# Performance work log

Measured on AMD Instinct MI355X. Metric: run time of the kernel, lower is better.

## Reference

```python
import jax, jax.numpy as jnp
import numpy as np

EMBED_DIM = 1024
NUM_HEADS = 16
N_QUBITS = 4
CIRCUIT_DEPTH = 2


def setup_inputs() -> dict:
    key = jax.random.key(0)
    ks = jax.random.split(key, 6)
    B, S, E = 2, 2048, EMBED_DIM
    x = jax.random.normal(ks[0], (B, S, E), dtype=jnp.float32)
    Wq = jax.random.normal(ks[1], (E, E), dtype=jnp.float32) / np.sqrt(E)
    Wk = jax.random.normal(ks[2], (E, E), dtype=jnp.float32) / np.sqrt(E)
    Wv = jax.random.normal(ks[3], (E, E), dtype=jnp.float32) / np.sqrt(E)
    Wo = jax.random.normal(ks[4], (E, E), dtype=jnp.float32) / np.sqrt(E)
    q_params = jax.random.normal(ks[5], (N_QUBITS, CIRCUIT_DEPTH), dtype=jnp.float32)
    return {"x": x, "Wq": Wq, "Wk": Wk, "Wv": Wv, "Wo": Wo, "q_params": q_params}


def reference(x, Wq, Wk, Wv, Wo, q_params):
    B, S, E = x.shape
    H, dk = NUM_HEADS, E // NUM_HEADS
    # QKV projections (Linear, no bias): y = x @ W.T
    q = (x @ Wq.T).reshape(B, S, H, dk).transpose(0, 2, 1, 3)  # [B,H,S,dk]
    k = (x @ Wk.T).reshape(B, S, H, dk).transpose(0, 2, 1, 3)
    v = (x @ Wv.T).reshape(B, S, H, dk).transpose(0, 2, 1, 3)
    scores = jnp.einsum("bhqd,bhkd->bhqk", q, k) / jnp.sqrt(jnp.float32(dk))
    attn = jax.nn.softmax(scores, axis=-1)
    classical = jnp.einsum("bhqk,bhkd->bhqd", attn, v)  # [B,H,S,dk]
    # Quantum circuit collapses analytically: RX-only circuit, <Z_0> depends
    # only on the rotations on wire 0 -> cos(sum_depth q_params[0, :]).
    c = jnp.cos(jnp.sum(q_params[0, :]))
    mixed = classical.at[..., :N_QUBITS].add(c)
    mixed = mixed.transpose(0, 2, 1, 3).reshape(B, S, E)
    return mixed @ Wo.T
```

## Files before the change

### kernel.cpp

```cpp
#include <hip/hip_runtime.h>

typedef unsigned short u16;
typedef unsigned int u32;
typedef __attribute__((ext_vector_type(8))) short short8;
typedef __attribute__((ext_vector_type(8))) _Float16 half8;
typedef __attribute__((ext_vector_type(4))) float f32x4;
typedef __attribute__((ext_vector_type(16))) float f32x16;
typedef __attribute__((ext_vector_type(4))) u32 u32x4;

#define S_LEN 2048
#define EDIM  1024
#define DK    64
#define NHEAD 16
#define QSCALE 0.1803368801111f

__device__ inline u16 f2bf(float f) {
    u32 u = __builtin_bit_cast(u32, f);
    u += 0x7fffu + ((u >> 16) & 1u);
    return (u16)(u >> 16);
}
__device__ inline u16 f2h(float f) {
    _Float16 h = (_Float16)f;
    return __builtin_bit_cast(u16, h);
}

#define ASYNC16(gp, lp)                                                        \
    __builtin_amdgcn_global_load_lds(                                          \
        (const __attribute__((address_space(1))) u32*)(gp),                    \
        (__attribute__((address_space(3))) u32*)(lp), 16, 0, 0)

__global__ __launch_bounds__(256)
void conv_all(const float* __restrict__ x,  const float* __restrict__ Wq,
              const float* __restrict__ Wk, const float* __restrict__ Wv,
              u16* __restrict__ xb, u16* __restrict__ Wb ) {
    const int blk = blockIdx.x;
    const float* src; u16* dst; int idx;
    if (blk < 4096)      { src = x;  dst = xb;             idx = blk; }
    else if (blk < 5120) { src = Wq; dst = Wb;             idx = blk - 4096; }
    else if (blk < 6144) { src = Wk; dst = Wb + (1 << 20); idx = blk - 5120; }
    else                 { src = Wv; dst = Wb + (2 << 20); idx = blk - 6144; }
    const int i = idx * 1024 + threadIdx.x * 4;
    const float4 v = *(const float4*)(src + i);
    u16 o[4] = { f2bf(v.x), f2bf(v.y), f2bf(v.z), f2bf(v.w) };
    *(ulong1*)(dst + i) = *(ulong1*)o;
}

__global__ __launch_bounds__(256)
void f32_to_bf16(const float* __restrict__ src, u16* __restrict__ dst, int n) {
    const int i = (blockIdx.x * 256 + threadIdx.x) * 4;
    if (i + 3 < n) {
        const float4 v = *(const float4*)(src + i);
        u16 o[4] = { f2bf(v.x), f2bf(v.y), f2bf(v.z), f2bf(v.w) };
        *(ulong1*)(dst + i) = *(ulong1*)o;
    }
}

template<int EPI, bool BF32, int MT>
__global__ __launch_bounds__(256, 2)
void gemm128(const u16* __restrict__ A,
             const void* __restrict__ B0, const void* __restrict__ B1,
             const void* __restrict__ B2,
             u16* __restrict__ C0, u16* __restrict__ C1, u16* __restrict__ C2,
             float* __restrict__ Cf, int M, int N, int K) {
    const void* Bv = B0;
    u16*        Cp = C0;
    float       cscale = (EPI == 0) ? QSCALE : 1.0f;
    if (blockIdx.z == 1) { Bv = B1; Cp = C1; cscale = 1.0f; }
    else if (blockIdx.z == 2) { Bv = B2; Cp = C2; cscale = 1.0f; }

    const int tid  = threadIdx.x;
    const int lane = tid & 63;
    const int w    = tid >> 6;
    const int quad = lane >> 4;
    const int l16  = lane & 15;
    const int wm   = w >> 1;
    const int wn   = w & 1;
    const int m0   = blockIdx.y * (MT * 32);
    const int n0   = blockIdx.x * 128;

    __shared__ u16 lA[MT * 32 * 32];
    __shared__ __align__(16) char lBraw[BF32 ? 128 * 32 * 4 : 128 * 32 * 2];

    f32x4 acc[MT][4] = {};

    for (int k0 = 0; k0 < K; k0 += 32) {
        __syncthreads();
#pragma unroll
        for (int i = 0; i < MT / 2; ++i) {
            const int row = w * (MT * 8) + i * 16 + (lane >> 2);
            const int col = (lane & 3) * 8;
            ASYNC16(A + (size_t)(m0 + row) * K + k0 + col,
                    &lA[(w * (MT * 8) + i * 16) * 32]);
        }
        if (BF32) {
            const float* Bp = (const float*)Bv;
            float*       lB = (float*)lBraw;
#pragma unroll
            for (int i = 0; i < 4; ++i) {
                const int row = w * 32 + i * 8 + (lane >> 3);
                const int col = (lane & 7) * 4;
                ASYNC16(Bp + (size_t)(n0 + row) * K + k0 + col,
                        &lB[(w * 32 + i * 8) * 32]);
            }
        } else {
            const u16* Bp = (const u16*)Bv;
            u16*       lB = (u16*)lBraw;
#pragma unroll
            for (int i = 0; i < 2; ++i) {
                const int row = w * 32 + i * 16 + (lane >> 2);
                const int col = (lane & 3) * 8;
                ASYNC16(Bp + (size_t)(n0 + row) * K + k0 + col,
                        &lB[(w * 32 + i * 16) * 32]);
            }
        }
        __syncthreads();

        short8 av[MT], bv[4];
#pragma unroll
        for (int t = 0; t < MT; ++t)
            av[t] = *(const short8*)&lA[(wm * (MT * 16) + t * 16 + l16) * 32 + quad * 8];
        if (BF32) {
            const float* lB = (const float*)lBraw;
#pragma unroll
            for (int t = 0; t < 4; ++t) {
                const float* src = &lB[(wn * 64 + t * 16 + l16) * 32 + quad * 8];
                const f32x4 x0 = *(const f32x4*)src;
                const f32x4 x1 = *(const f32x4*)(src + 4);
                short8 bq;
#pragma unroll
                for (int j = 0; j < 4; ++j) {
                    bq[j]     = (short)f2bf(x0[j]);
                    bq[4 + j] = (short)f2bf(x1[j]);
                }
                bv[t] = bq;
            }
        } else {
            const u16* lB = (const u16*)lBraw;
#pragma unroll
            for (int t = 0; t < 4; ++t)
                bv[t] = *(const short8*)&lB[(wn * 64 + t * 16 + l16) * 32 + quad * 8];
        }

#pragma unroll
        for (int mt = 0; mt < MT; ++mt)
#pragma unroll
            for (int nt = 0; nt < 4; ++nt)
                acc[mt][nt] = __builtin_amdgcn_mfma_f32_16x16x32_bf16(
                    av[mt], bv[nt], acc[mt][nt], 0, 0, 0);
    }

#pragma unroll
    for (int mt = 0; mt < MT; ++mt)
#pragma unroll
        for (int nt = 0; nt < 4; ++nt) {
            if (EPI == 0 && blockIdx.z == 2) {
                const int col  = n0 + wn * 64 + nt * 16 + l16;
                const int h    = (col >> 6) & 15;
                const int d    = col & 63;
                const int rowb = m0 + wm * (MT * 16) + mt * 16 + quad * 4;
                const int b    = rowb >> 11;
                const int s    = rowb & 2047;
                ushort4 o;
                o.x = f2h(acc[mt][nt][0]);
                o.y = f2h(acc[mt][nt][1]);
                o.z = f2h(acc[mt][nt][2]);
                o.w = f2h(acc[mt][nt][3]);
                *(ushort4*)&Cp[((size_t)(b * 16 + h) * 64 + d) * S_LEN + s] = o;
            } else {
#pragma unroll
                for (int r = 0; r < 4; ++r) {
                    const int row = m0 + wm * (MT * 16) + mt * 16 + quad * 4 + r;
                    const int col = n0 + wn * 64 + nt * 16 + l16;
                    if (EPI == 2)
                        Cf[(size_t)row * N + col] = acc[mt][nt][r];
                    else
                        Cp[(size_t)row * N + col] = f2bf(acc[mt][nt][r] * cscale);
                }
            }
        }
}

__global__ __launch_bounds__(256, 2)
void attn5(const u16* __restrict__ Qg, const u16* __restrict__ Kg,
           const u16* __restrict__ VTg , const float* __restrict__ qp,
           u16* __restrict__ Mg) {
    const int tid  = threadIdx.x;
    const int lane = tid & 63;
    const int w    = tid >> 6;
    const int l32  = lane & 31;
    const int hi   = lane >> 5;
    const int bh   = blockIdx.x;
    const int b    = bh >> 4;
    const int h    = bh & 15;
    const int q0   = blockIdx.y * 128;

    __shared__ u16 lK[2][128 * 64];
    __shared__ u16 lV[2][64 * 128];

    const float qc = cosf(qp[0] + qp[1]);

    short8 bq[4];
    {
        const u16* qrow = Qg + (size_t)(b * S_LEN + q0 + w * 32 + l32) * EDIM +
                          h * DK + hi * 8;
#pragma unroll
        for (int kk = 0; kk < 4; ++kk)
            bq[kk] = *(const short8*)(qrow + kk * 16);
    }

    const int kpiece = (lane & 7) ^ ((lane >> 3) & 7);
    const u16* kgbase = Kg + (size_t)b * S_LEN * EDIM + h * DK + kpiece * 8 +
                        (size_t)(w * 32 + (lane >> 3)) * EDIM;
    const u16* vgbase = VTg + (size_t)(bh * DK + w * 16 + (lane >> 4)) * S_LEN;

    f32x16 oacc[2] = {};
    float  li = 0.f;

#define STAGE(BUF, J0)                                                         \
    {                                                                          \
        _Pragma("unroll")                                                      \
        for (int i = 0; i < 4; ++i)                                            \
            ASYNC16(kgbase + (size_t)(J0 + i * 8) * EDIM,                      \
                    &lK[BUF][(w * 32 + i * 8) * 64]);                          \
        _Pragma("unroll")                                                      \
        for (int i = 0; i < 4; ++i) {                                          \
            const int pv = (lane & 15) ^ ((w * 16 + i * 4 + (lane >> 4)) & 15);\
            ASYNC16(vgbase + (size_t)(i * 4) * S_LEN + (J0) + pv * 8,          \
                    &lV[BUF][(w * 16 + i * 4) * 128]);                         \
        }                                                                      \
    }

    STAGE(0, 0)

    for (int t = 0; t < S_LEN / 128; ++t) {
        __syncthreads();
        if (t + 1 < S_LEN / 128)
            STAGE((t + 1) & 1, (t + 1) * 128)
        const u16* bK = lK[t & 1];
        const u16* bVb = lV[t & 1];

#pragma unroll
        for (int jt = 0; jt < 4; ++jt) {
            const int jr = jt * 32 + l32;
            f32x16 sT = {};
#pragma unroll
            for (int kk = 0; kk < 4; ++kk) {
                const short8 aK = *(const short8*)
                    &bK[jr * 64 + ((kk * 2 + hi) ^ (l32 & 7)) * 8];
                sT = __builtin_amdgcn_mfma_f32_32x32x16_bf16(aK, bq[kk], sT, 0, 0, 0);
            }
            float e[16];
#pragma unroll
            for (int r = 0; r < 16; ++r) {
                e[r] = __builtin_amdgcn_exp2f(sT[r]);
                li += e[r];
            }
#pragma unroll
            for (int s = 0; s < 2; ++s) {
                const u32 P0 = __builtin_bit_cast(u32,
                    __builtin_amdgcn_cvt_pkrtz(e[8 * s + 0], e[8 * s + 1]));
                const u32 P1 = __builtin_bit_cast(u32,
                    __builtin_amdgcn_cvt_pkrtz(e[8 * s + 2], e[8 * s + 3]));
                const u32 P2 = __builtin_bit_cast(u32,
                    __builtin_amdgcn_cvt_pkrtz(e[8 * s + 4], e[8 * s + 5]));
                const u32 P3 = __builtin_bit_cast(u32,
                    __builtin_amdgcn_cvt_pkrtz(e[8 * s + 6], e[8 * s + 7]));
                const u32 XA = (u32)__shfl_xor((int)(hi ? P0 : P2), 32, 64);
                const u32 XB = (u32)__shfl_xor((int)(hi ? P1 : P3), 32, 64);
                u32x4 tt;
                tt[0] = hi ? XA : P0;
                tt[1] = hi ? XB : P1;
                tt[2] = hi ? P2 : XA;
                tt[3] = hi ? P3 : XB;
                const half8 aP = __builtin_bit_cast(half8, tt);
                const int ks = jt * 2 + s;
#pragma unroll
                for (int dt = 0; dt < 2; ++dt) {
                    const int d = dt * 32 + l32;
                    const half8 bV = *(const half8*)
                        &bVb[d * 128 + ((ks * 2 + hi) ^ (l32 & 15)) * 8];
                    oacc[dt] = __builtin_amdgcn_mfma_f32_32x32x16_f16(
                        aP, bV, oacc[dt], 0, 0, 0);
                }
            }
        }
    }
#undef STAGE

    li += __shfl_xor(li, 32, 64);
    const float inv = 1.f / li;
#pragma unroll
    for (int r = 0; r < 16; ++r) {
        const int ml   = (r & 3) + 8 * (r >> 2) + 4 * hi;
        const float im = __shfl(inv, ml, 64);
        const int sg   = q0 + w * 32 + ml;
#pragma unroll
        for (int dt = 0; dt < 2; ++dt) {
            const int d = dt * 32 + l32;
            float val = oacc[dt][r] * im;
            if (d < 4) val += qc;
            Mg[(size_t)(b * S_LEN + sg) * EDIM + h * DK + d] = f2bf(val);
        }
    }
}

extern "C" void kernel_launch(void* const* d_in, const int* in_sizes, int n_in,
                              void* d_out, int out_size, void* d_ws, size_t ws_size,
                              hipStream_t stream) {
    const float* x  = (const float*)d_in[0];
    const float* Wq = (const float*)d_in[1];
    const float* Wk = (const float*)d_in[2];
    const float* Wv = (const float*)d_in[3];
    const float* Wo = (const float*)d_in[4];
    const float* qp = (const float*)d_in[5];

    const size_t BUF  = (size_t)2 * S_LEN * EDIM;
    const size_t WBUF = (size_t)EDIM * EDIM;

    u16* Q  = (u16*)d_out;
    u16* Kb = Q + BUF;

    u16* ws    = (u16*)d_ws;
    u16* xb    = ws;
    u16* mixed = xb;
    u16* VT    = ws + BUF;
    u16* Wqb   = ws + 2 * BUF;
    u16* Wkb   = Wqb + WBUF;
    u16* Wvb   = Wkb + WBUF;
    u16* Wob   = Wqb;
    float* out = (float*)d_out;

    const int M = 2 * S_LEN, N = EDIM, Kd = EDIM;
    const dim3 gqkv(N / 128, M / 128, 3);
    const dim3 gfin(N / 128, M / 64, 1);
    const dim3 gattn(2 * NHEAD, S_LEN / 128, 1);
    const bool fast = ws_size >= (size_t)(2 * BUF + 3 * WBUF) * sizeof(u16);

    if (fast) {
        conv_all<<<7168, 256, 0, stream>>>(x, Wq, Wk, Wv, xb, Wqb);
        gemm128<0, false, 4><<<gqkv, 256, 0, stream>>>(
            xb, Wqb, Wkb, Wvb, Q, Kb, VT, nullptr, M, N, Kd);
        f32_to_bf16<<<(int)(WBUF / 1024), 256, 0, stream>>>(Wo, Wob, (int)WBUF);
        attn5<<<gattn, 256, 0, stream>>>(Q, Kb, VT, qp, mixed);
        gemm128<2, false, 2><<<gfin, 256, 0, stream>>>(
            mixed, Wob, Wob, Wob, nullptr, nullptr, nullptr, out, M, N, Kd);
    } else {
        f32_to_bf16<<<(int)(BUF / 1024), 256, 0, stream>>>(x, xb, (int)BUF);
        gemm128<0, true, 4><<<gqkv, 256, 0, stream>>>(
            xb, Wq, Wk, Wv, Q, Kb, VT, nullptr, M, N, Kd);
        attn5<<<gattn, 256, 0, stream>>>(Q, Kb, VT, qp, mixed);
        gemm128<2, true, 2><<<gfin, 256, 0, stream>>>(
            mixed, Wo, Wo, Wo, nullptr, nullptr, nullptr, out, M, N, Kd);
    }
}
```

Baseline: 187.4 us.

## Use K=64 swizzled LDS tiles in GEMM and drop P shuffles in attention

After: 170.2 us. 1.1x faster.

```diff
diff --git a/kernel.cpp b/kernel.cpp
--- a/kernel.cpp
+++ b/kernel.cpp
@@ -78,52 +78,80 @@
     const int m0   = blockIdx.y * (MT * 32);
     const int n0   = blockIdx.x * 128;
 
-    __shared__ u16 lA[MT * 32 * 32];
-    __shared__ __align__(16) char lBraw[BF32 ? 128 * 32 * 4 : 128 * 32 * 2];
+    __shared__ u16 lA[MT * 32 * (BF32 ? 32 : 64)];
+    __shared__ __align__(16) char lBraw[BF32 ? 128 * 32 * 4 : 128 * 64 * 2];
 
     f32x4 acc[MT][4] = {};
 
-    for (int k0 = 0; k0 < K; k0 += 32) {
-        __syncthreads();
-#pragma unroll
-        for (int i = 0; i < MT / 2; ++i) {
-            const int row = w * (MT * 8) + i * 16 + (lane >> 2);
-            const int col = (lane & 3) * 8;
-            ASYNC16(A + (size_t)(m0 + row) * K + k0 + col,
-                    &lA[(w * (MT * 8) + i * 16) * 32]);
-        }
-        if (BF32) {
-            const float* Bp = (const float*)Bv;
-            float*       lB = (float*)lBraw;
+    if (!BF32) {
+        u16* lB = (u16*)lBraw;
+        const int rsub  = lane >> 3;
+        const int piece = (lane & 7) ^ (rsub & 7);
+        for (int k0 = 0; k0 < K; k0 += 64) {
+            __syncthreads();
+#pragma unroll
+            for (int i = 0; i < MT; ++i) {
+                const int row = w * (MT * 8) + i * 8 + rsub;
+                ASYNC16(A + (size_t)(m0 + row) * K + k0 + piece * 8,
+                        &lA[(w * (MT * 8) + i * 8) * 64]);
+            }
+            const u16* Bp = (const u16*)Bv;
+#pragma unroll
+            for (int i = 0; i < 4; ++i) {
+                const int row = w * 32 + i * 8 + rsub;
+                ASYNC16(Bp + (size_t)(n0 + row) * K + k0 + piece * 8,
+                        &lB[(w * 32 + i * 8) * 64]);
+            }
+            __syncthreads();
+
+#pragma unroll
+            for (int ks = 0; ks < 2; ++ks) {
+                short8 av[MT], bv[4];
+#pragma unroll
+                for (int t = 0; t < MT; ++t)
+                    av[t] = *(const short8*)&lA[(wm * (MT * 16) + t * 16 + l16) * 64 +
+                                                (((ks * 4 + quad)) ^ (l16 & 7)) * 8];
+#pragma unroll
+                for (int t = 0; t < 4; ++t)
+                    bv[t] = *(const short8*)&lB[(wn * 64 + t * 16 + l16) * 64 +
+                                                (((ks * 4 + quad)) ^ (l16 & 7)) * 8];
+#pragma unroll
+                for (int mt = 0; mt < MT; ++mt)
+#pragma unroll
+                    for (int nt = 0; nt < 4; ++nt)
+                        acc[mt][nt] = __builtin_amdgcn_mfma_f32_16x16x32_bf16(
+                            av[mt], bv[nt], acc[mt][nt], 0, 0, 0);
+            }
+        }
+    } else {
+        for (int k0 = 0; k0 < K; k0 += 32) {
+            __syncthreads();
+#pragma unroll
+            for (int i = 0; i < MT / 2; ++i) {
+                const int row = w * (MT * 8) + i * 16 + (lane >> 2);
+                const int col = (lane & 3) * 8;
+                ASYNC16(A + (size_t)(m0 + row) * K + k0 + col,
+                        &lA[(w * (MT * 8) + i * 16) * 32]);
+            }
+            const float* Bp  = (const float*)Bv;
+            float*       lBs = (float*)lBraw;
 #pragma unroll
             for (int i = 0; i < 4; ++i) {
                 const int row = w * 32 + i * 8 + (lane >> 3);
                 const int col = (lane & 7) * 4;
                 ASYNC16(Bp + (size_t)(n0 + row) * K + k0 + col,
-                        &lB[(w * 32 + i * 8) * 32]);
-            }
-        } else {
-            const u16* Bp = (const u16*)Bv;
-            u16*       lB = (u16*)lBraw;
-#pragma unroll
-            for (int i = 0; i < 2; ++i) {
-                const int row = w * 32 + i * 16 + (lane >> 2);
-                const int col = (lane & 3) * 8;
-                ASYNC16(Bp + (size_t)(n0 + row) * K + k0 + col,
-                        &lB[(w * 32 + i * 16) * 32]);
-            }
-        }
-        __syncthreads();
-
-        short8 av[MT], bv[4];
-#pragma unroll
-        for (int t = 0; t < MT; ++t)
-            av[t] = *(const short8*)&lA[(wm * (MT * 16) + t * 16 + l16) * 32 + quad * 8];
-        if (BF32) {
-            const float* lB = (const float*)lBraw;
+                        &lBs[(w * 32 + i * 8) * 32]);
+            }
+            __syncthreads();
+
+            short8 av[MT], bv[4];
+#pragma unroll
+            for (int t = 0; t < MT; ++t)
+                av[t] = *(const short8*)&lA[(wm * (MT * 16) + t * 16 + l16) * 32 + quad * 8];
+            const float* lBr = (const float*)lBraw;
 #pragma unroll
             for (int t = 0; t < 4; ++t) {
-                const float* src = &lB[(wn * 64 + t * 16 + l16) * 32 + quad * 8];
+                const float* src = &lBr[(wn * 64 + t * 16 + l16) * 32 + quad * 8];
                 const f32x4 x0 = *(const f32x4*)src;
                 const f32x4 x1 = *(const f32x4*)(src + 4);
                 short8 bq;
@@ -134,19 +162,13 @@
                 }
                 bv[t] = bq;
             }
-        } else {
-            const u16* lB = (const u16*)lBraw;
-#pragma unroll
-            for (int t = 0; t < 4; ++t)
-                bv[t] = *(const short8*)&lB[(wn * 64 + t * 16 + l16) * 32 + quad * 8];
-        }
-
-#pragma unroll
-        for (int mt = 0; mt < MT; ++mt)
-#pragma unroll
-            for (int nt = 0; nt < 4; ++nt)
-                acc[mt][nt] = __builtin_amdgcn_mfma_f32_16x16x32_bf16(
-                    av[mt], bv[nt], acc[mt][nt], 0, 0, 0);
+#pragma unroll
+            for (int mt = 0; mt < MT; ++mt)
+#pragma unroll
+                for (int nt = 0; nt < 4; ++nt)
+                    acc[mt][nt] = __builtin_amdgcn_mfma_f32_16x16x32_bf16(
+                        av[mt], bv[nt], acc[mt][nt], 0, 0, 0);
+        }
     }
 
 #pragma unroll
@@ -154,12 +176,13 @@
 #pragma unroll
         for (int nt = 0; nt < 4; ++nt) {
             if (EPI == 0 && blockIdx.z == 2) {
-                const int col  = n0 + wn * 64 + nt * 16 + l16;
-                const int h    = (col >> 6) & 15;
-                const int d    = col & 63;
-                const int rowb = m0 + wm * (MT * 16) + mt * 16 + quad * 4;
-                const int b    = rowb >> 11;
-                const int s    = rowb & 2047;
+                const int col    = n0 + wn * 64 + nt * 16 + l16;
+                const int h      = (col >> 6) & 15;
+                const int d      = col & 63;
+                const int quadsw = ((quad & 1) << 1) | (quad >> 1);
+                const int rowb   = m0 + wm * (MT * 16) + mt * 16;
+                const int b      = rowb >> 11;
+                const int s      = (rowb & 2047) + quadsw * 4;
                 ushort4 o;
                 o.x = f2h(acc[mt][nt][0]);
                 o.y = f2h(acc[mt][nt][1]);
@@ -181,9 +204,9 @@
 }
 
 __global__ __launch_bounds__(256, 2)
-void attn5(const u16* __restrict__ Qg, const u16* __restrict__ Kg,
-           const u16* __restrict__ VTg , const float* __restrict__ qp,
-           u16* __restrict__ Mg) {
+void attn6(const u16* __restrict__ Qg, const u16* __restrict__ Kg,
+           const u16* __restrict__ VTg ,
+           const float* __restrict__ qp, u16* __restrict__ Mg) {
     const int tid  = threadIdx.x;
     const int lane = tid & 63;
     const int w    = tid >> 6;
@@ -213,8 +236,8 @@
                         (size_t)(w * 32 + (lane >> 3)) * EDIM;
     const u16* vgbase = VTg + (size_t)(bh * DK + w * 16 + (lane >> 4)) * S_LEN;
 
-    f32x16 oacc[2] = {};
-    float  li = 0.f;
+    f32x16 oacc[2][2] = {};
+    float  la[4] = {};
 
 #define STAGE(BUF, J0)                                                         \
     {                                                                          \
@@ -236,7 +259,7 @@
         __syncthreads();
         if (t + 1 < S_LEN / 128)
             STAGE((t + 1) & 1, (t + 1) * 128)
-        const u16* bK = lK[t & 1];
+        const u16* bK  = lK[t & 1];
         const u16* bVb = lV[t & 1];
 
 #pragma unroll
@@ -253,25 +276,19 @@
 #pragma unroll
             for (int r = 0; r < 16; ++r) {
                 e[r] = __builtin_amdgcn_exp2f(sT[r]);
-                li += e[r];
+                la[r & 3] += e[r];
             }
 #pragma unroll
             for (int s = 0; s < 2; ++s) {
-                const u32 P0 = __builtin_bit_cast(u32,
+                u32x4 tt;
+                tt[0] = __builtin_bit_cast(u32,
                     __builtin_amdgcn_cvt_pkrtz(e[8 * s + 0], e[8 * s + 1]));
-                const u32 P1 = __builtin_bit_cast(u32,
+                tt[1] = __builtin_bit_cast(u32,
                     __builtin_amdgcn_cvt_pkrtz(e[8 * s + 2], e[8 * s + 3]));
-                const u32 P2 = __builtin_bit_cast(u32,
+                tt[2] = __builtin_bit_cast(u32,
                     __builtin_amdgcn_cvt_pkrtz(e[8 * s + 4], e[8 * s + 5]));
-                const u32 P3 = __builtin_bit_cast(u32,
+                tt[3] = __builtin_bit_cast(u32,
                     __builtin_amdgcn_cvt_pkrtz(e[8 * s + 6], e[8 * s + 7]));
-                const u32 XA = (u32)__shfl_xor((int)(hi ? P0 : P2), 32, 64);
-                const u32 XB = (u32)__shfl_xor((int)(hi ? P1 : P3), 32, 64);
-                u32x4 tt;
-                tt[0] = hi ? XA : P0;
-                tt[1] = hi ? XB : P1;
-                tt[2] = hi ? P2 : XA;
-                tt[3] = hi ? P3 : XB;
                 const half8 aP = __builtin_bit_cast(half8, tt);
                 const int ks = jt * 2 + s;
 #pragma unroll
@@ -279,14 +296,15 @@
                     const int d = dt * 32 + l32;
                     const half8 bV = *(const half8*)
                         &bVb[d * 128 + ((ks * 2 + hi) ^ (l32 & 15)) * 8];
-                    oacc[dt] = __builtin_amdgcn_mfma_f32_32x32x16_f16(
-                        aP, bV, oacc[dt], 0, 0, 0);
+                    oacc[s][dt] = __builtin_amdgcn_mfma_f32_32x32x16_f16(
+                        aP, bV, oacc[s][dt], 0, 0, 0);
                 }
             }
         }
     }
 #undef STAGE
 
+    float li = (la[0] + la[1]) + (la[2] + la[3]);
     li += __shfl_xor(li, 32, 64);
     const float inv = 1.f / li;
 #pragma unroll
@@ -297,7 +315,7 @@
 #pragma unroll
         for (int dt = 0; dt < 2; ++dt) {
             const int d = dt * 32 + l32;
-            float val = oacc[dt][r] * im;
+            float val = (oacc[0][dt][r] + oacc[1][dt][r]) * im;
             if (d < 4) val += qc;
             Mg[(size_t)(b * S_LEN + sg) * EDIM + h * DK + d] = f2bf(val);
         }
@@ -341,14 +359,14 @@
         gemm128<0, false, 4><<<gqkv, 256, 0, stream>>>(
             xb, Wqb, Wkb, Wvb, Q, Kb, VT, nullptr, M, N, Kd);
         f32_to_bf16<<<(int)(WBUF / 1024), 256, 0, stream>>>(Wo, Wob, (int)WBUF);
-        attn5<<<gattn, 256, 0, stream>>>(Q, Kb, VT, qp, mixed);
+        attn6<<<gattn, 256, 0, stream>>>(Q, Kb, VT, qp, mixed);
         gemm128<2, false, 2><<<gfin, 256, 0, stream>>>(
             mixed, Wob, Wob, Wob, nullptr, nullptr, nullptr, out, M, N, Kd);
     } else {
         f32_to_bf16<<<(int)(BUF / 1024), 256, 0, stream>>>(x, xb, (int)BUF);
         gemm128<0, true, 4><<<gqkv, 256, 0, stream>>>(
             xb, Wq, Wk, Wv, Q, Kb, VT, nullptr, M, N, Kd);
-        attn5<<<gattn, 256, 0, stream>>>(Q, Kb, VT, qp, mixed);
+        attn6<<<gattn, 256, 0, stream>>>(Q, Kb, VT, qp, mixed);
         gemm128<2, true, 2><<<gfin, 256, 0, stream>>>(
             mixed, Wo, Wo, Wo, nullptr, nullptr, nullptr, out, M, N, Kd);
     }
```
